# Kernel optimization log

Measured on AMD Instinct MI355X. Metric: run time of the kernel, lower is better.

The kernel has to match this reference:

```python
import jax, jax.numpy as jnp
import numpy as np

B, H, T, N, DK = 4, 8, 12, 325, 32


def setup_inputs() -> dict:
    key = jax.random.key(0)
    ks = jax.random.split(key, 8)
    shp = (B, H, T, N, DK)
    return {
        "Qf": jax.random.normal(ks[0], shp, jnp.float32),
        "Kf": jax.random.normal(ks[1], shp, jnp.float32),
        "Vf": jax.random.normal(ks[2], shp, jnp.float32),
        "Qs": jax.random.normal(ks[3], shp, jnp.float32),
        "Ks": jax.random.normal(ks[4], shp, jnp.float32),
        "Vs": jax.random.normal(ks[5], shp, jnp.float32),
        "Kj": jax.random.normal(ks[6], (N, 1), jnp.float32),   # FlowSpeed jam density param
        "Vf_p": jax.random.normal(ks[7], (N, 1), jnp.float32),  # FlowSpeed free-flow speed param
    }


def reference(Qf, Kf, Vf, Qs, Ks, Vs, Kj, Vf_p):
    d_k = Qf.shape[-1]
    scale = 1.0 / np.sqrt(d_k).astype(np.float32)

    # FlowSpeed nonlinearity: flow = Kj * (speed - speed^2 / (Vf + 1e-5))
    # Kj, Vf_p: (N,1) broadcast over (..., N, d_k)
    Qf_from_speed = Kj * (Qs - jnp.square(Qs) / (Vf_p + 1e-5))

    def attn(q, k, v):
        # q,k,v: [B,H,T,N,dk]; scores: [B,H,T,N,N]
        scores = jnp.einsum("bhtnd,bhtmd->bhtnm", q, k) * scale
        return jnp.einsum("bhtnm,bhtmd->bhtnd", jax.nn.softmax(scores, axis=-1), v)

    context_flow_flow = attn(Qf, Kf, Vf)
    context_flow_speed = attn(Kf, Qf_from_speed, Vf)
    context_speed_flow = attn(Ks, Qf, Vs)
    context_speed_speed = attn(Qs, Ks, Vs)
    return (context_flow_flow, context_flow_speed, context_speed_flow, context_speed_speed)
```

## Files before the change

### kernel.cpp

```cpp
#include <hip/hip_runtime.h>
#include <hip/hip_bf16.h>

typedef float f32x4 __attribute__((ext_vector_type(4)));
typedef short short8 __attribute__((ext_vector_type(8)));

#define NT    325
#define DKK   32
#define NSL   384
#define SLICE (NT*DKK)
#define TOTE  (NSL*SLICE)
#define NKT   21
#define PADV  352
#define VGRAN (32 * (PADV/8))
#define SCALE2 0.25506372f

__device__ __forceinline__ int swz(int sidx, int row) { return sidx ^ ((row & 7) << 3); }

__device__ __forceinline__ unsigned cvtpk(float lo, float hi) {
    unsigned r;
    asm("v_cvt_pk_bf16_f32 %0, %1, %2" : "=v"(r) : "v"(lo), "v"(hi));
    return r;
}
__device__ __forceinline__ unsigned pk2_split(float x, float y, unsigned& lopk) {
    const unsigned hi = cvtpk(x, y);
    const float hx = __builtin_bit_cast(float, hi << 16);
    const float hy = __builtin_bit_cast(float, hi & 0xffff0000u);
    lopk = cvtpk(x - hx, y - hy);
    return hi;
}
__device__ __forceinline__ void swap32(unsigned& a, unsigned& b) {
    asm("v_permlane32_swap_b32 %0, %1" : "+v"(a), "+v"(b));
}
__device__ __forceinline__ void swap16(unsigned& a, unsigned& b) {
    asm("v_permlane16_swap_b32 %0, %1" : "+v"(a), "+v"(b));
}
__device__ __forceinline__ short8 repack(const f32x4& a0, const f32x4& a1, bool hasB) {
    unsigned u = cvtpk(a0[0], a0[1]);
    unsigned v = cvtpk(a0[2], a0[3]);
    unsigned s = hasB ? cvtpk(a1[0], a1[1]) : 0u;
    unsigned t = hasB ? cvtpk(a1[2], a1[3]) : 0u;
    swap32(u, s); swap16(u, s);
    swap32(v, t); swap16(v, t);
    uint4 w; w.x = u; w.y = v; w.z = s; w.w = t;
    return __builtin_bit_cast(short8, w);
}

__global__ __launch_bounds__(512, 3)
void attn_slim(const float* __restrict__ Qf, const float* __restrict__ Kf,
               const float* __restrict__ Vf, const float* __restrict__ Qs,
               const float* __restrict__ Ks, const float* __restrict__ Vs,
               float* __restrict__ out)
{
    __shared__ __align__(16) unsigned short Kb[336 * DKK];
    __shared__ __align__(16) unsigned short Vt[DKK * PADV];

    const int tid = threadIdx.x;
    const int bid = blockIdx.x;
    const int bt  = bid / 3;
    const int vr  = bid - 3 * bt;
    const int vi  = (vr + bt) % 3;
    const int var = (vi == 0) ? 0 : (vi == 1) ? 2 : 3;
    const size_t base = (size_t)bt * SLICE;

    const float *qp, *kp, *vp;
    if      (var == 0) { qp = Qf; kp = Kf; vp = Vf; }
    else if (var == 2) { qp = Ks; kp = Qf; vp = Vs; }
    else               { qp = Qs; kp = Ks; vp = Vs; }
    float* op = out + (size_t)var * TOTE + base;

    for (int i8 = tid; i8 < SLICE / 8; i8 += 512) {
        const int idx = i8 * 8;
        const int m   = idx >> 5;
        const float* s = kp + base + idx;
        const float4 a = *(const float4*)s;
        const float4 b = *(const float4*)(s + 4);
        uint4 pkv;
        pkv.x = cvtpk(a.x, a.y); pkv.y = cvtpk(a.z, a.w);
        pkv.z = cvtpk(b.x, b.y); pkv.w = cvtpk(b.z, b.w);
        *(uint4*)&Kb[swz(idx, m)] = pkv;
    }

    for (int gi = tid; gi < VGRAN; gi += 512) {
        const int dd = gi & 31;
        const int m8 = gi >> 5;
        const int mb = m8 * 8;
        float v[8];
        #pragma unroll
        for (int i = 0; i < 8; ++i) {
            const int m = mb + i;
            v[i] = (m < NT) ? vp[base + (size_t)m * DKK + dd] : 0.0f;
        }
        uint4 pkv;
        pkv.x = cvtpk(v[0], v[1]); pkv.y = cvtpk(v[2], v[3]);
        pkv.z = cvtpk(v[4], v[5]); pkv.w = cvtpk(v[6], v[7]);
        *(uint4*)&Vt[swz(dd * PADV + mb, dd)] = pkv;
    }
    __syncthreads();

    const int lane = tid & 63;
    const int wv   = tid >> 6;
    const int c    = lane & 15;
    const int g    = lane >> 4;
    const int kswz = (c & 7) << 3;
    const f32x4 zero = {0.f, 0.f, 0.f, 0.f};

    int qt = wv;
    float4 qa, qb;
    {
        int qr = qt * 16 + c; if (qr > NT - 1) qr = NT - 1;
        const float* s = qp + base + (size_t)qr * DKK + g * 8;
        qa = *(const float4*)s; qb = *(const float4*)(s + 4);
    }

    for (; qt < NKT; qt += 8) {
        float4 na, nb;
        const bool more = (qt + 8) < NKT;
        if (more) {
            int qr = (qt + 8) * 16 + c; if (qr > NT - 1) qr = NT - 1;
            const float* s = qp + base + (size_t)qr * DKK + g * 8;
            na = *(const float4*)s; nb = *(const float4*)(s + 4);
        }

        uint4 qwh;
        qwh.x = cvtpk(qa.x * SCALE2, qa.y * SCALE2);
        qwh.y = cvtpk(qa.z * SCALE2, qa.w * SCALE2);
        qwh.z = cvtpk(qb.x * SCALE2, qb.y * SCALE2);
        qwh.w = cvtpk(qb.z * SCALE2, qb.w * SCALE2);
        const short8 qh = __builtin_bit_cast(short8, qwh);

        f32x4 o0a = zero, o1a = zero, o0b = zero, o1b = zero;
        float ts0 = 0.f, ts1 = 0.f, ts2 = 0.f, ts3 = 0.f;

        #pragma unroll
        for (int ks = 0; ks < 11; ++ks) {
            const int fi0 = (((2 * ks) * 16 + c) * DKK + g * 8) ^ kswz;
            const int fi1 = fi0 + 16 * DKK;
            const bool hasB1 = (ks < 10);
            f32x4 a0, a1;

            __builtin_amdgcn_s_setprio(1);
            {
                const short8 k0 = *(const short8*)&Kb[fi0];
                a0 = __builtin_amdgcn_mfma_f32_16x16x32_bf16(k0, qh, zero, 0, 0, 0);
                if (hasB1) {
                    const short8 k1 = *(const short8*)&Kb[fi1];
                    a1 = __builtin_amdgcn_mfma_f32_16x16x32_bf16(k1, qh, zero, 0, 0, 0);
                }
            }
            __builtin_amdgcn_s_setprio(0);

            if (ks == 10) {
                #pragma unroll
                for (int r = 0; r < 4; ++r)
                    a0[r] = (4 * g + r > 4) ? -1e30f : a0[r];
            }

            a0[0] = exp2f(a0[0]); a0[1] = exp2f(a0[1]);
            a0[2] = exp2f(a0[2]); a0[3] = exp2f(a0[3]);
            ts0 += a0[0]; ts1 += a0[1]; ts2 += a0[2]; ts3 += a0[3];
            if (hasB1) {
                a1[0] = exp2f(a1[0]); a1[1] = exp2f(a1[1]);
                a1[2] = exp2f(a1[2]); a1[3] = exp2f(a1[3]);
                ts0 += a1[0]; ts1 += a1[1]; ts2 += a1[2]; ts3 += a1[3];
            }

            const short8 af = repack(a0, hasB1 ? a1 : a0, hasB1);
            const short8 v0 = *(const short8*)&Vt[( c        * PADV + ks * 32 + g * 8) ^ kswz];
            const short8 v1 = *(const short8*)&Vt[((c + 16)  * PADV + ks * 32 + g * 8) ^ kswz];
            __builtin_amdgcn_s_setprio(1);
            if (ks & 1) {
                o0b = __builtin_amdgcn_mfma_f32_16x16x32_bf16(af, v0, o0b, 0, 0, 0);
                o1b = __builtin_amdgcn_mfma_f32_16x16x32_bf16(af, v1, o1b, 0, 0, 0);
            } else {
                o0a = __builtin_amdgcn_mfma_f32_16x16x32_bf16(af, v0, o0a, 0, 0, 0);
                o1a = __builtin_amdgcn_mfma_f32_16x16x32_bf16(af, v1, o1a, 0, 0, 0);
            }
            __builtin_amdgcn_s_setprio(0);
        }

        float ts = (ts0 + ts1) + (ts2 + ts3);
        ts += __shfl_xor(ts, 16);
        ts += __shfl_xor(ts, 32);
        const float inv = 1.0f / ts;
        const f32x4 o0 = o0a + o0b;
        const f32x4 o1 = o1a + o1b;

        #pragma unroll
        for (int r = 0; r < 4; ++r) {
            const int row = qt * 16 + 4 * g + r;
            const float iv = __shfl(inv, 4 * g + r);
            if (row < NT) {
                op[(size_t)row * DKK + c]      = o0[r] * iv;
                op[(size_t)row * DKK + c + 16] = o1[r] * iv;
            }
        }
        qa = na; qb = nb;
    }
}

__global__ __launch_bounds__(512, 2)
void attn_fat(const float* __restrict__ Kf, const float* __restrict__ Vf,
              const float* __restrict__ Qs,
              const float* __restrict__ Kj, const float* __restrict__ Vfp,
              float* __restrict__ out)
{
    __shared__ __align__(16) unsigned short Kb[336 * DKK];
    __shared__ __align__(16) unsigned short Kl[336 * DKK];
    __shared__ __align__(16) unsigned short Vt[DKK * PADV];

    const int tid = threadIdx.x;
    const int bt  = blockIdx.x;
    const size_t base = (size_t)bt * SLICE;

    const float* qp = Kf;
    const float* kp = Qs;
    const float* vp = Vf;
    float* op = out + (size_t)1 * TOTE + base;

    for (int i8 = tid; i8 < SLICE / 8; i8 += 512) {
        const int idx = i8 * 8;
        const int m   = idx >> 5;
        const int sidx = swz(idx, m);
        const float* s = kp + base + idx;
        float4 a = *(const float4*)s;
        float4 b = *(const float4*)(s + 4);
        const float kj = Kj[m];
        const float rv = 1.0f / (Vfp[m] + 1e-5f);
        a.x = kj * (a.x - a.x * a.x * rv);
        a.y = kj * (a.y - a.y * a.y * rv);
        a.z = kj * (a.z - a.z * a.z * rv);
        a.w = kj * (a.w - a.w * a.w * rv);
        b.x = kj * (b.x - b.x * b.x * rv);
        b.y = kj * (b.y - b.y * b.y * rv);
        b.z = kj * (b.z - b.z * b.z * rv);
        b.w = kj * (b.w - b.w * b.w * rv);
        uint4 hw, lw;
        hw.x = pk2_split(a.x, a.y, lw.x);
        hw.y = pk2_split(a.z, a.w, lw.y);
        hw.z = pk2_split(b.x, b.y, lw.z);
        hw.w = pk2_split(b.z, b.w, lw.w);
        *(uint4*)&Kb[sidx] = hw;
        *(uint4*)&Kl[sidx] = lw;
    }

    for (int gi = tid; gi < VGRAN; gi += 512) {
        const int dd = gi & 31;
        const int m8 = gi >> 5;
        const int mb = m8 * 8;
        float v[8];
        #pragma unroll
        for (int i = 0; i < 8; ++i) {
            const int m = mb + i;
            v[i] = (m < NT) ? vp[base + (size_t)m * DKK + dd] : 0.0f;
        }
        uint4 pkv;
        pkv.x = cvtpk(v[0], v[1]); pkv.y = cvtpk(v[2], v[3]);
        pkv.z = cvtpk(v[4], v[5]); pkv.w = cvtpk(v[6], v[7]);
        *(uint4*)&Vt[swz(dd * PADV + mb, dd)] = pkv;
    }
    __syncthreads();

    const int lane = tid & 63;
    const int wv   = tid >> 6;
    const int c    = lane & 15;
    const int g    = lane >> 4;
    const int kswz = (c & 7) << 3;
    const f32x4 zero = {0.f, 0.f, 0.f, 0.f};

    int qt = wv;
    float4 qa, qb;
    {
        int qr = qt * 16 + c; if (qr > NT - 1) qr = NT - 1;
        const float* s = qp + base + (size_t)qr * DKK + g * 8;
        qa = *(const float4*)s; qb = *(const float4*)(s + 4);
    }

    for (; qt < NKT; qt += 8) {
        float4 na, nb;
        const bool more = (qt + 8) < NKT;
        if (more) {
            int qr = (qt + 8) * 16 + c; if (qr > NT - 1) qr = NT - 1;
            const float* s = qp + base + (size_t)qr * DKK + g * 8;
            na = *(const float4*)s; nb = *(const float4*)(s + 4);
        }

        uint4 qwh, qwl;
        qwh.x = pk2_split(qa.x * SCALE2, qa.y * SCALE2, qwl.x);
        qwh.y = pk2_split(qa.z * SCALE2, qa.w * SCALE2, qwl.y);
        qwh.z = pk2_split(qb.x * SCALE2, qb.y * SCALE2, qwl.z);
        qwh.w = pk2_split(qb.z * SCALE2, qb.w * SCALE2, qwl.w);
        const short8 qh = __builtin_bit_cast(short8, qwh);
        const short8 ql = __builtin_bit_cast(short8, qwl);

        f32x4 o0a = zero, o1a = zero, o0b = zero, o1b = zero;
        float ts0 = 0.f, ts1 = 0.f, ts2 = 0.f, ts3 = 0.f;
        float mrow = -1e30f;

        #pragma unroll
        for (int ks = 0; ks < 11; ++ks) {
            const int fi0 = (((2 * ks) * 16 + c) * DKK + g * 8) ^ kswz;
            const int fi1 = fi0 + 16 * DKK;
            const bool hasB1 = (ks < 10);
            f32x4 a0, a1;

            __builtin_amdgcn_s_setprio(1);
            {
                const short8 kh = *(const short8*)&Kb[fi0];
                const short8 kl = *(const short8*)&Kl[fi0];
                f32x4 t = __builtin_amdgcn_mfma_f32_16x16x32_bf16(kh, ql, zero, 0, 0, 0);
                t = __builtin_amdgcn_mfma_f32_16x16x32_bf16(kl, qh, t, 0, 0, 0);
                a0 = __builtin_amdgcn_mfma_f32_16x16x32_bf16(kh, qh, t, 0, 0, 0);
            }
            if (hasB1) {
                const short8 kh = *(const short8*)&Kb[fi1];
                const short8 kl = *(const short8*)&Kl[fi1];
                f32x4 t = __builtin_amdgcn_mfma_f32_16x16x32_bf16(kh, ql, zero, 0, 0, 0);
                t = __builtin_amdgcn_mfma_f32_16x16x32_bf16(kl, qh, t, 0, 0, 0);
                a1 = __builtin_amdgcn_mfma_f32_16x16x32_bf16(kh, qh, t, 0, 0, 0);
            }
            __builtin_amdgcn_s_setprio(0);

            if (ks == 10) {
                #pragma unroll
                for (int r = 0; r < 4; ++r)
                    a0[r] = (4 * g + r > 4) ? -1e30f : a0[r];
            }

            float pm = fmaxf(fmaxf(a0[0], a0[1]), fmaxf(a0[2], a0[3]));
            if (hasB1)
                pm = fmaxf(pm, fmaxf(fmaxf(a1[0], a1[1]), fmaxf(a1[2], a1[3])));
            pm = fmaxf(pm, __shfl_xor(pm, 16));
            pm = fmaxf(pm, __shfl_xor(pm, 32));
            if (__any(pm > mrow)) {
                const float mn = fmaxf(mrow, pm);
                const float f = exp2f(mrow - mn);
                mrow = mn;
                ts0 *= f; ts1 *= f; ts2 *= f; ts3 *= f;
                #pragma unroll
                for (int r = 0; r < 4; ++r) {
                    const float fr = __shfl(f, 4 * g + r);
                    o0a[r] *= fr; o1a[r] *= fr;
                    o0b[r] *= fr; o1b[r] *= fr;
                }
            }
            a0[0] = exp2f(a0[0] - mrow); a0[1] = exp2f(a0[1] - mrow);
            a0[2] = exp2f(a0[2] - mrow); a0[3] = exp2f(a0[3] - mrow);
            ts0 += a0[0]; ts1 += a0[1]; ts2 += a0[2]; ts3 += a0[3];
            if (hasB1) {
                a1[0] = exp2f(a1[0] - mrow); a1[1] = exp2f(a1[1] - mrow);
                a1[2] = exp2f(a1[2] - mrow); a1[3] = exp2f(a1[3] - mrow);
                ts0 += a1[0]; ts1 += a1[1]; ts2 += a1[2]; ts3 += a1[3];
            }

            const short8 af = repack(a0, hasB1 ? a1 : a0, hasB1);
            const short8 v0 = *(const short8*)&Vt[( c        * PADV + ks * 32 + g * 8) ^ kswz];
            const short8 v1 = *(const short8*)&Vt[((c + 16)  * PADV + ks * 32 + g * 8) ^ kswz];
            __builtin_amdgcn_s_setprio(1);
            if (ks & 1) {
                o0b = __builtin_amdgcn_mfma_f32_16x16x32_bf16(af, v0, o0b, 0, 0, 0);
                o1b = __builtin_amdgcn_mfma_f32_16x16x32_bf16(af, v1, o1b, 0, 0, 0);
            } else {
                o0a = __builtin_amdgcn_mfma_f32_16x16x32_bf16(af, v0, o0a, 0, 0, 0);
                o1a = __builtin_amdgcn_mfma_f32_16x16x32_bf16(af, v1, o1a, 0, 0, 0);
            }
            __builtin_amdgcn_s_setprio(0);
        }

        float ts = (ts0 + ts1) + (ts2 + ts3);
        ts += __shfl_xor(ts, 16);
        ts += __shfl_xor(ts, 32);
        const float inv = 1.0f / ts;
        const f32x4 o0 = o0a + o0b;
        const f32x4 o1 = o1a + o1b;

        #pragma unroll
        for (int r = 0; r < 4; ++r) {
            const int row = qt * 16 + 4 * g + r;
            const float iv = __shfl(inv, 4 * g + r);
            if (row < NT) {
                op[(size_t)row * DKK + c]      = o0[r] * iv;
                op[(size_t)row * DKK + c + 16] = o1[r] * iv;
            }
        }
        qa = na; qb = nb;
    }
}

extern "C" void kernel_launch(void* const* d_in, const int* in_sizes, int n_in,
                              void* d_out, int out_size, void* d_ws, size_t ws_size,
                              hipStream_t stream) {
    const float* Qf  = (const float*)d_in[0];
    const float* Kf  = (const float*)d_in[1];
    const float* Vf  = (const float*)d_in[2];
    const float* Qs  = (const float*)d_in[3];
    const float* Ks  = (const float*)d_in[4];
    const float* Vs  = (const float*)d_in[5];
    const float* Kj  = (const float*)d_in[6];
    const float* Vfp = (const float*)d_in[7];
    float* out = (float*)d_out;

    attn_slim<<<dim3(NSL * 3), dim3(512), 0, stream>>>(Qf, Kf, Vf, Qs, Ks, Vs, out);
    attn_fat <<<dim3(NSL),     dim3(512), 0, stream>>>(Kf, Vf, Qs, Kj, Vfp, out);
}
```

Before: 102.5 us.

## Switch slim attention kernel to 32x32x16 MFMA tiles with 32-row query tiles

The slim attention kernel now processes 32-row query tiles using 32x32x16 bf16 MFMA instructions instead of 16-row tiles with 16x16x32 MFMAs. The K buffer is padded to 352 rows and zero-filled so whole 32-key blocks can be read, and the softmax repack and row-sum shuffle are adapted to the 32x32 accumulator layout. The goal is fewer MFMA and LDS-load instructions per unit of work and more K/V reuse per wave. In exchange only 11 query tiles are spread over 8 waves, so load is uneven, register pressure per wave is higher (16-wide accumulators), and the previous prefetch of the next Q tile is dropped.

```diff
diff --git a/kernel.cpp b/kernel.cpp
--- a/kernel.cpp
+++ b/kernel.cpp
@@ -1,7 +1,8 @@
 #include <hip/hip_runtime.h>
 #include <hip/hip_bf16.h>
 
-typedef float f32x4 __attribute__((ext_vector_type(4)));
+typedef float f32x4  __attribute__((ext_vector_type(4)));
+typedef float f32x16 __attribute__((ext_vector_type(16)));
 typedef short short8 __attribute__((ext_vector_type(8)));
 
 #define NT    325
@@ -10,6 +11,7 @@
 #define SLICE (NT*DKK)
 #define TOTE  (NSL*SLICE)
 #define NKT   21
+#define NQT32 11
 #define PADV  352
 #define VGRAN (32 * (PADV/8))
 #define SCALE2 0.25506372f
@@ -51,7 +53,7 @@
                const float* __restrict__ Ks, const float* __restrict__ Vs,
                float* __restrict__ out)
 {
-    __shared__ __align__(16) unsigned short Kb[336 * DKK];
+    __shared__ __align__(16) unsigned short Kb[PADV * DKK];
     __shared__ __align__(16) unsigned short Vt[DKK * PADV];
 
     const int tid = threadIdx.x;
@@ -68,15 +70,19 @@
     else               { qp = Qs; kp = Ks; vp = Vs; }
     float* op = out + (size_t)var * TOTE + base;
 
-    for (int i8 = tid; i8 < SLICE / 8; i8 += 512) {
+    for (int i8 = tid; i8 < (PADV * DKK) / 8; i8 += 512) {
         const int idx = i8 * 8;
         const int m   = idx >> 5;
-        const float* s = kp + base + idx;
-        const float4 a = *(const float4*)s;
-        const float4 b = *(const float4*)(s + 4);
         uint4 pkv;
-        pkv.x = cvtpk(a.x, a.y); pkv.y = cvtpk(a.z, a.w);
-        pkv.z = cvtpk(b.x, b.y); pkv.w = cvtpk(b.z, b.w);
+        if (m < NT) {
+            const float* s = kp + base + idx;
+            const float4 a = *(const float4*)s;
+            const float4 b = *(const float4*)(s + 4);
+            pkv.x = cvtpk(a.x, a.y); pkv.y = cvtpk(a.z, a.w);
+            pkv.z = cvtpk(b.x, b.y); pkv.w = cvtpk(b.z, b.w);
+        } else {
+            pkv.x = pkv.y = pkv.z = pkv.w = 0u;
+        }
         *(uint4*)&Kb[swz(idx, m)] = pkv;
     }
 
@@ -99,102 +105,95 @@
 
     const int lane = tid & 63;
     const int wv   = tid >> 6;
-    const int c    = lane & 15;
-    const int g    = lane >> 4;
-    const int kswz = (c & 7) << 3;
-    const f32x4 zero = {0.f, 0.f, 0.f, 0.f};
-
-    int qt = wv;
-    float4 qa, qb;
-    {
-        int qr = qt * 16 + c; if (qr > NT - 1) qr = NT - 1;
-        const float* s = qp + base + (size_t)qr * DKK + g * 8;
-        qa = *(const float4*)s; qb = *(const float4*)(s + 4);
-    }
-
-    for (; qt < NKT; qt += 8) {
-        float4 na, nb;
-        const bool more = (qt + 8) < NKT;
-        if (more) {
-            int qr = (qt + 8) * 16 + c; if (qr > NT - 1) qr = NT - 1;
-            const float* s = qp + base + (size_t)qr * DKK + g * 8;
-            na = *(const float4*)s; nb = *(const float4*)(s + 4);
-        }
-
-        uint4 qwh;
-        qwh.x = cvtpk(qa.x * SCALE2, qa.y * SCALE2);
-        qwh.y = cvtpk(qa.z * SCALE2, qa.w * SCALE2);
-        qwh.z = cvtpk(qb.x * SCALE2, qb.y * SCALE2);
-        qwh.w = cvtpk(qb.z * SCALE2, qb.w * SCALE2);
-        const short8 qh = __builtin_bit_cast(short8, qwh);
-
-        f32x4 o0a = zero, o1a = zero, o0b = zero, o1b = zero;
+    const int l31  = lane & 31;
+    const int h    = lane >> 5;
+    const int d0   = h * 8;
+    const int swz8 = (lane & 7) << 3;
+    const f32x16 zero16 = {0,0,0,0,0,0,0,0,0,0,0,0,0,0,0,0};
+
+    for (int qt = wv; qt < NQT32; qt += 8) {
+        int qr = qt * 32 + l31; if (qr > NT - 1) qr = NT - 1;
+        const float* qsrc = qp + base + (size_t)qr * DKK;
+        const float4 qA = *(const float4*)(qsrc + d0);
+        const float4 qB = *(const float4*)(qsrc + d0 + 4);
+        const float4 qC = *(const float4*)(qsrc + 16 + d0);
+        const float4 qD = *(const float4*)(qsrc + 16 + d0 + 4);
+        uint4 w1, w2;
+        w1.x = cvtpk(qA.x * SCALE2, qA.y * SCALE2);
+        w1.y = cvtpk(qA.z * SCALE2, qA.w * SCALE2);
+        w1.z = cvtpk(qB.x * SCALE2, qB.y * SCALE2);
+        w1.w = cvtpk(qB.z * SCALE2, qB.w * SCALE2);
+        w2.x = cvtpk(qC.x * SCALE2, qC.y * SCALE2);
+        w2.y = cvtpk(qC.z * SCALE2, qC.w * SCALE2);
+        w2.z = cvtpk(qD.x * SCALE2, qD.y * SCALE2);
+        w2.w = cvtpk(qD.z * SCALE2, qD.w * SCALE2);
+        const short8 q1 = __builtin_bit_cast(short8, w1);
+        const short8 q2 = __builtin_bit_cast(short8, w2);
+
+        f32x16 o = zero16;
         float ts0 = 0.f, ts1 = 0.f, ts2 = 0.f, ts3 = 0.f;
 
         #pragma unroll
-        for (int ks = 0; ks < 11; ++ks) {
-            const int fi0 = (((2 * ks) * 16 + c) * DKK + g * 8) ^ kswz;
-            const int fi1 = fi0 + 16 * DKK;
-            const bool hasB1 = (ks < 10);
-            f32x4 a0, a1;
+        for (int ks = 0; ks < NQT32; ++ks) {
+            const int mrow = ks * 32 + l31;
+            const int ki1 = (mrow * DKK + d0) ^ swz8;
+            const int ki2 = (mrow * DKK + 16 + d0) ^ swz8;
+            const short8 k1 = *(const short8*)&Kb[ki1];
+            const short8 k2 = *(const short8*)&Kb[ki2];
 
             __builtin_amdgcn_s_setprio(1);
-            {
-                const short8 k0 = *(const short8*)&Kb[fi0];
-                a0 = __builtin_amdgcn_mfma_f32_16x16x32_bf16(k0, qh, zero, 0, 0, 0);
-                if (hasB1) {
-                    const short8 k1 = *(const short8*)&Kb[fi1];
-                    a1 = __builtin_amdgcn_mfma_f32_16x16x32_bf16(k1, qh, zero, 0, 0, 0);
-                }
-            }
+            f32x16 a = __builtin_amdgcn_mfma_f32_32x32x16_bf16(k1, q1, zero16, 0, 0, 0);
+            a = __builtin_amdgcn_mfma_f32_32x32x16_bf16(k2, q2, a, 0, 0, 0);
             __builtin_amdgcn_s_setprio(0);
 
             if (ks == 10) {
                 #pragma unroll
-                for (int r = 0; r < 4; ++r)
-                    a0[r] = (4 * g + r > 4) ? -1e30f : a0[r];
-            }
-
-            a0[0] = exp2f(a0[0]); a0[1] = exp2f(a0[1]);
-            a0[2] = exp2f(a0[2]); a0[3] = exp2f(a0[3]);
-            ts0 += a0[0]; ts1 += a0[1]; ts2 += a0[2]; ts3 += a0[3];
-            if (hasB1) {
-                a1[0] = exp2f(a1[0]); a1[1] = exp2f(a1[1]);
-                a1[2] = exp2f(a1[2]); a1[3] = exp2f(a1[3]);
-                ts0 += a1[0]; ts1 += a1[1]; ts2 += a1[2]; ts3 += a1[3];
-            }
-
-            const short8 af = repack(a0, hasB1 ? a1 : a0, hasB1);
-            const short8 v0 = *(const short8*)&Vt[( c        * PADV + ks * 32 + g * 8) ^ kswz];
-            const short8 v1 = *(const short8*)&Vt[((c + 16)  * PADV + ks * 32 + g * 8) ^ kswz];
+                for (int r = 0; r < 16; ++r) {
+                    const int ml = (r & 3) + 8 * (r >> 2) + 4 * h;
+                    a[r] = (ml > 4) ? -1e30f : a[r];
+                }
+            }
+
+            #pragma unroll
+            for (int r = 0; r < 16; ++r) a[r] = exp2f(a[r]);
+            ts0 += (a[0] + a[1]) + (a[2] + a[3]);
+            ts1 += (a[4] + a[5]) + (a[6] + a[7]);
+            ts2 += (a[8] + a[9]) + (a[10] + a[11]);
+            ts3 += (a[12] + a[13]) + (a[14] + a[15]);
+
+            unsigned u1 = cvtpk(a[0],  a[1]),  v1w = cvtpk(a[2],  a[3]);
+            unsigned s1 = cvtpk(a[4],  a[5]),  t1  = cvtpk(a[6],  a[7]);
+            swap32(u1, s1); swap32(v1w, t1);
+            uint4 wa; wa.x = u1; wa.y = v1w; wa.z = s1; wa.w = t1;
+            const short8 af1 = __builtin_bit_cast(short8, wa);
+            unsigned u2 = cvtpk(a[8],  a[9]),  v2w = cvtpk(a[10], a[11]);
+            unsigned s2 = cvtpk(a[12], a[13]), t2  = cvtpk(a[14], a[15]);
+            swap32(u2, s2); swap32(v2w, t2);
+            uint4 wb; wb.x = u2; wb.y = v2w; wb.z = s2; wb.w = t2;
+            const short8 af2 = __builtin_bit_cast(short8, wb);
+
+            const int vi1 = (l31 * PADV + ks * 32 + d0) ^ swz8;
+            const int vi2 = (l31 * PADV + ks * 32 + 16 + d0) ^ swz8;
+            const short8 vf1 = *(const short8*)&Vt[vi1];
+            const short8 vf2 = *(const short8*)&Vt[vi2];
+
             __builtin_amdgcn_s_setprio(1);
-            if (ks & 1) {
-                o0b = __builtin_amdgcn_mfma_f32_16x16x32_bf16(af, v0, o0b, 0, 0, 0);
-                o1b = __builtin_amdgcn_mfma_f32_16x16x32_bf16(af, v1, o1b, 0, 0, 0);
-            } else {
-                o0a = __builtin_amdgcn_mfma_f32_16x16x32_bf16(af, v0, o0a, 0, 0, 0);
-                o1a = __builtin_amdgcn_mfma_f32_16x16x32_bf16(af, v1, o1a, 0, 0, 0);
-            }
+            o = __builtin_amdgcn_mfma_f32_32x32x16_bf16(af1, vf1, o, 0, 0, 0);
+            o = __builtin_amdgcn_mfma_f32_32x32x16_bf16(af2, vf2, o, 0, 0, 0);
             __builtin_amdgcn_s_setprio(0);
         }
 
         float ts = (ts0 + ts1) + (ts2 + ts3);
-        ts += __shfl_xor(ts, 16);
         ts += __shfl_xor(ts, 32);
         const float inv = 1.0f / ts;
-        const f32x4 o0 = o0a + o0b;
-        const f32x4 o1 = o1a + o1b;
-
-        #pragma unroll
-        for (int r = 0; r < 4; ++r) {
-            const int row = qt * 16 + 4 * g + r;
-            const float iv = __shfl(inv, 4 * g + r);
-            if (row < NT) {
-                op[(size_t)row * DKK + c]      = o0[r] * iv;
-                op[(size_t)row * DKK + c + 16] = o1[r] * iv;
-            }
-        }
-        qa = na; qb = nb;
+
+        #pragma unroll
+        for (int r = 0; r < 16; ++r) {
+            const int ql  = (r & 3) + 8 * (r >> 2) + 4 * h;
+            const int row = qt * 32 + ql;
+            const float iv = __shfl(inv, ql);
+            if (row < NT) op[(size_t)row * DKK + l31] = o[r] * iv;
+        }
     }
 }
 
```

Result: slower. 268.3 us (+161.7%).
